# Kernel optimization log

Measured on AMD Instinct MI355X. Metric: run time of the kernel, lower is better.

## Reference

```python
import jax, jax.numpy as jnp
import numpy as np

N_HEAD = 8
D_K = 64
D_V = 512
TOP_K = 64
NEG = jnp.finfo(jnp.float32).min


def setup_inputs() -> dict:
    key = jax.random.key(0)
    ks = jax.random.split(key, 10)
    B, Lq, Lk, E = 2, 2048, 2048, 512
    q = jax.random.normal(ks[0], (B, Lq, E), dtype=jnp.float32)
    k = jax.random.normal(ks[1], (B, Lk, E), dtype=jnp.float32)
    v = jax.random.normal(ks[2], (B, Lk, D_V), dtype=jnp.float32)
    post_softmax_mask = jax.random.randint(ks[3], (B, 1, Lq, Lk), 0, 2, dtype=jnp.int32)
    query_mask_flat = jax.random.uniform(ks[4], (B, Lq), dtype=jnp.float32)
    # Linear weights stored input-major: y = x @ W
    Wq = jax.random.normal(ks[5], (E, N_HEAD * D_K), dtype=jnp.float32) * (E ** -0.5)
    Wk = jax.random.normal(ks[6], (E, N_HEAD * D_K), dtype=jnp.float32) * (E ** -0.5)
    Wv = jax.random.normal(ks[7], (D_V, N_HEAD * D_V), dtype=jnp.float32) * (D_V ** -0.5)
    Wfc = jax.random.normal(ks[8], (N_HEAD * D_V, D_V), dtype=jnp.float32) * ((N_HEAD * D_V) ** -0.5)
    return {"q": q, "k": k, "v": v, "post_softmax_mask": post_softmax_mask,
            "query_mask_flat": query_mask_flat, "Wq": Wq, "Wk": Wk, "Wv": Wv, "Wfc": Wfc}


def _topk_keep_mask(logits, top_k):
    # Scatter True at the per-row top-k indices (matches torch.topk + scatter_).
    B, H, Lq, Lk = logits.shape
    _, idx = jax.lax.top_k(logits, top_k)              # [B,H,Lq,K]
    rows = B * H * Lq
    keep = jnp.zeros((rows, Lk), dtype=bool)
    keep = keep.at[jnp.arange(rows)[:, None], idx.reshape(rows, top_k)].set(True)
    return keep.reshape(B, H, Lq, Lk)


def reference(q, k, v, post_softmax_mask, query_mask_flat, Wq, Wk, Wv, Wfc):
    B, Lq, _ = q.shape
    Lk = k.shape[1]
    q_proj = (q @ Wq).reshape(B, Lq, N_HEAD, D_K).transpose(0, 2, 1, 3)   # [B,H,Lq,dk]
    k_proj = (k @ Wk).reshape(B, Lk, N_HEAD, D_K).transpose(0, 2, 1, 3)   # [B,H,Lk,dk]
    logits = jnp.einsum('bhqd,bhkd->bhqk', q_proj * (D_K ** -0.5), k_proj).astype(jnp.float32)
    # post-softmax mask (applied pre-softmax via -inf fill, as in source)
    logits = jnp.where(post_softmax_mask == 0, NEG, logits)
    # top-k restriction, skipped for rows where query_mask_flat <= 0.5
    keep = _topk_keep_mask(logits, TOP_K)
    masked_queries = (query_mask_flat > 0.5)[:, None, :, None]            # [B,1,Lq,1]
    keep = jnp.where(masked_queries, keep, True)
    logits = jnp.where(keep, logits, NEG)
    attn_probs = jax.nn.softmax(logits, axis=-1).astype(v.dtype)          # [B,H,Lq,Lk]
    v_proj = (v @ Wv).reshape(B, Lk, N_HEAD, D_V).transpose(0, 2, 1, 3)   # [B,H,Lk,dv]
    mixed = jnp.einsum('bhqk,bhkd->bhqd', attn_probs, v_proj)
    output = mixed.transpose(0, 2, 1, 3).reshape(B, Lq, N_HEAD * D_V) @ Wfc
    return output, attn_probs
```

## Files before the change

### kernel.cpp

```cpp
#include <hip/hip_runtime.h>
#include <stdint.h>

#define NEGF  (-3.402823466e38f)
#define TOPK  64

typedef __attribute__((ext_vector_type(8))) short bfrag8;
typedef __attribute__((ext_vector_type(4))) float f32x4;
typedef __attribute__((ext_vector_type(16))) float f32x16;

static __device__ __forceinline__ unsigned short f2bf(float f) {
  union { float f; unsigned u; } c; c.f = f;
  unsigned u = c.u;
  return (unsigned short)((u + 0x7fffu + ((u >> 16) & 1u)) >> 16);
}
static __device__ __forceinline__ unsigned mono(float x) {
  union { float f; unsigned u; } c; c.f = x;
  return (c.u & 0x80000000u) ? ~c.u : (c.u | 0x80000000u);
}
static __device__ __forceinline__ float invmono(unsigned k) {
  union { unsigned u; float f; } c;
  c.u = (k & 0x80000000u) ? (k ^ 0x80000000u) : ~k;
  return c.f;
}
static __device__ __forceinline__ int waveSum(int v) {
  #pragma unroll
  for (int o = 1; o < 64; o <<= 1) v += __shfl_xor(v, o);
  return v;
}
static __device__ __forceinline__ float waveSumF(float v) {
  #pragma unroll
  for (int o = 1; o < 64; o <<= 1) v += __shfl_xor(v, o);
  return v;
}
static __device__ __forceinline__ unsigned waveMaxU(unsigned v) {
  #pragma unroll
  for (int o = 1; o < 64; o <<= 1) {
    unsigned t = (unsigned)__shfl_xor((int)v, o);
    v = v > t ? v : t;
  }
  return v;
}

template<int OBF>
__global__ __launch_bounds__(256) void transpose_k(const float* __restrict__ in,
                                                   void* __restrict__ out, int R, int C) {
  __shared__ float t[32][33];
  int c0 = blockIdx.x * 32, r0 = blockIdx.y * 32;
  int tx = threadIdx.x & 31, ty = (threadIdx.x >> 5) * 4;
  #pragma unroll
  for (int i = 0; i < 4; i++)
    t[ty + i][tx] = in[(size_t)(r0 + ty + i) * C + c0 + tx];
  __syncthreads();
  #pragma unroll
  for (int i = 0; i < 4; i++) {
    float v = t[tx][ty + i];
    size_t idx = (size_t)(c0 + ty + i) * R + r0 + tx;
    if (OBF) ((unsigned short*)out)[idx] = f2bf(v);
    else     ((float*)out)[idx] = v;
  }
}

__global__ __launch_bounds__(256) void proj_f32_kernel(
    const float* __restrict__ q, const float* __restrict__ k,
    const float* __restrict__ WqT, const float* __restrict__ WkT,
    float* __restrict__ qp, float* __restrict__ kp) {
  __shared__ float AsT[64][132];
  __shared__ float BsT[64][132];
  int tid = threadIdx.x;
  int z = blockIdx.z;
  const float* A  = z ? k : q;
  const float* Bt = z ? WkT : WqT;
  float* out      = z ? kp : qp;
  float scale     = z ? 1.0f : 0.125f;
  int m0 = blockIdx.y * 128, n0 = blockIdx.x * 128;
  int lane = tid & 63, w = tid >> 6;
  int lx = lane & 15, ly = lane >> 4;
  int ra = w * 32 + ly * 4;
  int ca = lx * 4;
  int rr = tid >> 1;
  int kq0 = (tid & 1) << 5;
  float acc[8][8] = {};
  for (int k0 = 0; k0 < 512; k0 += 64) {
    const float* ar = A  + (size_t)(m0 + rr) * 512 + k0 + kq0;
    const float* br = Bt + (size_t)(n0 + rr) * 512 + k0 + kq0;
    #pragma unroll
    for (int s = 0; s < 8; s++) {
      float4 av = *(const float4*)(ar + (s << 2));
      float4 bv = *(const float4*)(br + (s << 2));
      int kk = kq0 + (s << 2);
      AsT[kk+0][rr] = av.x; AsT[kk+1][rr] = av.y; AsT[kk+2][rr] = av.z; AsT[kk+3][rr] = av.w;
      BsT[kk+0][rr] = bv.x; BsT[kk+1][rr] = bv.y; BsT[kk+2][rr] = bv.z; BsT[kk+3][rr] = bv.w;
    }
    __syncthreads();
    #pragma unroll 2
    for (int d = 0; d < 64; d++) {
      f32x4 a0 = *(const f32x4*)&AsT[d][ra];
      f32x4 a1 = *(const f32x4*)&AsT[d][ra + 16];
      f32x4 b0 = *(const f32x4*)&BsT[d][ca];
      f32x4 b1 = *(const f32x4*)&BsT[d][ca + 64];
      float a[8] = {a0[0],a0[1],a0[2],a0[3],a1[0],a1[1],a1[2],a1[3]};
      float bb[8] = {b0[0],b0[1],b0[2],b0[3],b1[0],b1[1],b1[2],b1[3]};
      #pragma unroll
      for (int i = 0; i < 8; i++)
        #pragma unroll
        for (int j = 0; j < 8; j++)
          acc[i][j] = fmaf(a[i], bb[j], acc[i][j]);
    }
    __syncthreads();
  }
  #pragma unroll
  for (int i = 0; i < 8; i++) {
    int m = m0 + ra + (i & 3) + ((i >> 2) << 4);
    int b = m >> 11, l = m & 2047;
    #pragma unroll
    for (int half = 0; half < 2; half++) {
      int n = n0 + ca + half * 64;
      int h = n >> 6, dd = n & 63;
      float4 v4;
      v4.x = acc[i][half*4+0]*scale; v4.y = acc[i][half*4+1]*scale;
      v4.z = acc[i][half*4+2]*scale; v4.w = acc[i][half*4+3]*scale;
      *(float4*)(out + ((((size_t)b*8 + h)*2048 + l)*64 + dd)) = v4;
    }
  }
}

__global__ __launch_bounds__(256) void logits_mask_kernel(
    const float* __restrict__ qp, const float* __restrict__ kp,
    const int* __restrict__ mask, float* __restrict__ out) {
  __shared__ float AsT[64][132];
  __shared__ float BsT[64][132];
  int tid = threadIdx.x;
  int z = blockIdx.z, b = z >> 3;
  int m0 = blockIdx.y * 128, n0 = blockIdx.x * 128;
  const float* Ap = qp + (size_t)z * (2048 * 64);
  const float* Bp = kp + (size_t)z * (2048 * 64);
  {
    int rr = tid >> 2;
    int kq = (tid & 3) << 2;
    #pragma unroll
    for (int pass = 0; pass < 2; pass++) {
      int r = rr + (pass << 6);
      const float* ar = Ap + (size_t)(m0 + r) * 64 + kq;
      const float* br = Bp + (size_t)(n0 + r) * 64 + kq;
      #pragma unroll
      for (int s = 0; s < 4; s++) {
        float4 av = *(const float4*)(ar + (s << 4));
        float4 bv = *(const float4*)(br + (s << 4));
        int k = kq + (s << 4);
        AsT[k+0][r] = av.x; AsT[k+1][r] = av.y; AsT[k+2][r] = av.z; AsT[k+3][r] = av.w;
        BsT[k+0][r] = bv.x; BsT[k+1][r] = bv.y; BsT[k+2][r] = bv.z; BsT[k+3][r] = bv.w;
      }
    }
  }
  __syncthreads();
  int lane = tid & 63, w = tid >> 6;
  int lx = lane & 15, ly = lane >> 4;
  int ra = w * 32 + ly * 4;
  int ca = lx * 4;
  float acc[8][8] = {};
  #pragma unroll 2
  for (int d = 0; d < 64; d++) {
    f32x4 a0 = *(const f32x4*)&AsT[d][ra];
    f32x4 a1 = *(const f32x4*)&AsT[d][ra + 16];
    f32x4 b0 = *(const f32x4*)&BsT[d][ca];
    f32x4 b1 = *(const f32x4*)&BsT[d][ca + 64];
    float a[8] = {a0[0],a0[1],a0[2],a0[3],a1[0],a1[1],a1[2],a1[3]};
    float bb[8] = {b0[0],b0[1],b0[2],b0[3],b1[0],b1[1],b1[2],b1[3]};
    #pragma unroll
    for (int i = 0; i < 8; i++)
      #pragma unroll
      for (int j = 0; j < 8; j++)
        acc[i][j] = fmaf(a[i], bb[j], acc[i][j]);
  }
  size_t outbase = (size_t)z * 2048 * 2048;
  const int* mbase = mask + (size_t)b * 2048 * 2048;
  #pragma unroll
  for (int i = 0; i < 8; i++) {
    int row = m0 + ra + (i & 3) + ((i >> 2) << 4);
    const int* mp = mbase + (size_t)row * 2048 + n0;
    float* op = out + outbase + (size_t)row * 2048 + n0;
    int4 mv0 = *(const int4*)(mp + ca);
    int4 mv1 = *(const int4*)(mp + ca + 64);
    float4 o0, o1;
    o0.x = mv0.x ? acc[i][0] : NEGF;
    o0.y = mv0.y ? acc[i][1] : NEGF;
    o0.z = mv0.z ? acc[i][2] : NEGF;
    o0.w = mv0.w ? acc[i][3] : NEGF;
    o1.x = mv1.x ? acc[i][4] : NEGF;
    o1.y = mv1.y ? acc[i][5] : NEGF;
    o1.z = mv1.z ? acc[i][6] : NEGF;
    o1.w = mv1.w ? acc[i][7] : NEGF;
    *(float4*)(op + ca) = o0;
    *(float4*)(op + ca + 64) = o1;
  }
}

__global__ __launch_bounds__(256) void vproj_kernel(const float* __restrict__ v,
    const unsigned short* __restrict__ WvT, unsigned short* __restrict__ vpT) {
  __shared__ unsigned short As[128][64];
  __shared__ unsigned short Bs[128][64];
  int tid = threadIdx.x;
  int lane = tid & 63, wv = tid >> 6;
  int l31 = lane & 31, lh = lane >> 5;
  int wr = wv >> 1, wc = wv & 1;
  int z = blockIdx.z, b = z >> 3, h = z & 7;
  int m0 = blockIdx.y * 128, n0 = blockIdx.x * 128;
  const unsigned short* Ap = WvT + (size_t)(h * 512 + m0) * 512;
  const float* Bp = v + ((size_t)b * 2048 + n0) * 512;
  f32x16 acc[2][2];
  #pragma unroll
  for (int mf = 0; mf < 2; mf++)
    #pragma unroll
    for (int nf = 0; nf < 2; nf++)
      #pragma unroll
      for (int r = 0; r < 16; r++) acc[mf][nf][r] = 0.f;
  int srow = tid >> 1;
  int skc = (tid & 1) << 5;
  for (int k0 = 0; k0 < 512; k0 += 64) {
    {
      const bfrag8* s = (const bfrag8*)(Ap + (size_t)srow * 512 + k0 + skc);
      #pragma unroll
      for (int j = 0; j < 4; j++) {
        int c = (skc >> 3) + j;
        *(bfrag8*)&As[srow][((c + srow) & 7) * 8] = s[j];
      }
    }
    {
      const float* s = Bp + (size_t)srow * 512 + k0 + skc;
      #pragma unroll
      for (int j = 0; j < 4; j++) {
        float4 x0 = *(const float4*)(s + 8*j);
        float4 x1 = *(const float4*)(s + 8*j + 4);
        union { bfrag8 v; unsigned short u[8]; } p;
        p.u[0]=f2bf(x0.x); p.u[1]=f2bf(x0.y); p.u[2]=f2bf(x0.z); p.u[3]=f2bf(x0.w);
        p.u[4]=f2bf(x1.x); p.u[5]=f2bf(x1.y); p.u[6]=f2bf(x1.z); p.u[7]=f2bf(x1.w);
        int c = (skc >> 3) + j;
        *(bfrag8*)&Bs[srow][((c + srow) & 7) * 8] = p.v;
      }
    }
    __syncthreads();
    #pragma unroll
    for (int ks = 0; ks < 4; ks++) {
      int qd = ks * 2 + lh;
      bfrag8 af[2], bfr[2];
      #pragma unroll
      for (int mf = 0; mf < 2; mf++) {
        int r = wr * 64 + mf * 32 + l31;
        af[mf] = *(const bfrag8*)&As[r][((qd + r) & 7) * 8];
      }
      #pragma unroll
      for (int nf = 0; nf < 2; nf++) {
        int n = wc * 64 + nf * 32 + l31;
        bfr[nf] = *(const bfrag8*)&Bs[n][((qd + n) & 7) * 8];
      }
      #pragma unroll
      for (int mf = 0; mf < 2; mf++)
        #pragma unroll
        for (int nf = 0; nf < 2; nf++)
          acc[mf][nf] = __builtin_amdgcn_mfma_f32_32x32x16_bf16(af[mf], bfr[nf], acc[mf][nf], 0, 0, 0);
    }
    __syncthreads();
  }
  #pragma unroll
  for (int mf = 0; mf < 2; mf++)
    #pragma unroll
    for (int nf = 0; nf < 2; nf++) {
      int l = n0 + wc * 64 + nf * 32 + l31;
      #pragma unroll
      for (int r = 0; r < 16; r++) {
        int d = m0 + wr * 64 + mf * 32 + (r & 3) + ((r >> 2) << 3) + (lh << 2);
        vpT[((size_t)z * 512 + d) * 2048 + l] = f2bf(acc[mf][nf][r]);
      }
    }
}

__global__ __launch_bounds__(256) void gemm_bf16_fc(const unsigned short* __restrict__ A,
    const unsigned short* __restrict__ Bt, float* __restrict__ Cout,
    int M, int N, int K) {
  __shared__ unsigned short As[64][72];
  __shared__ unsigned short Bs[128][72];
  int tid = threadIdx.x;
  int lane = tid & 63, wave = tid >> 6;
  int wr = wave >> 1, wc = wave & 1;
  int m0 = blockIdx.y * 64, n0 = blockIdx.x * 128;
  f32x4 acc[2][4];
  #pragma unroll
  for (int mi = 0; mi < 2; mi++)
    #pragma unroll
    for (int ni = 0; ni < 4; ni++) acc[mi][ni] = (f32x4){0.f, 0.f, 0.f, 0.f};
  int arow = tid >> 2, akc = (tid & 3) << 4;
  int brow = tid >> 1, bkc = (tid & 1) << 5;
  for (int k0 = 0; k0 < K; k0 += 64) {
    {
      const bfrag8* s = (const bfrag8*)(A + (size_t)(m0 + arow) * K + k0 + akc);
      *(bfrag8*)&As[arow][akc + 0] = s[0];
      *(bfrag8*)&As[arow][akc + 8] = s[1];
    }
    {
      const bfrag8* s = (const bfrag8*)(Bt + (size_t)(n0 + brow) * K + k0 + bkc);
      #pragma unroll
      for (int j = 0; j < 4; j++)
        *(bfrag8*)&Bs[brow][bkc + 8*j] = s[j];
    }
    __syncthreads();
    #pragma unroll
    for (int kh = 0; kh < 2; kh++) {
      int krd = (kh << 5) + ((lane >> 4) << 3);
      bfrag8 af[2], bfr[4];
      #pragma unroll
      for (int mi = 0; mi < 2; mi++)
        af[mi] = *(const bfrag8*)&As[wr*32 + mi*16 + (lane & 15)][krd];
      #pragma unroll
      for (int ni = 0; ni < 4; ni++)
        bfr[ni] = *(const bfrag8*)&Bs[wc*64 + ni*16 + (lane & 15)][krd];
      #pragma unroll
      for (int mi = 0; mi < 2; mi++)
        #pragma unroll
        for (int ni = 0; ni < 4; ni++)
          acc[mi][ni] = __builtin_amdgcn_mfma_f32_16x16x32_bf16(af[mi], bfr[ni], acc[mi][ni], 0, 0, 0);
    }
    __syncthreads();
  }
  #pragma unroll
  for (int mi = 0; mi < 2; mi++) {
    int rb = m0 + wr*32 + mi*16 + ((lane >> 4) << 2);
    #pragma unroll
    for (int ni = 0; ni < 4; ni++) {
      int col = n0 + wc*64 + ni*16 + (lane & 15);
      f32x4 v = acc[mi][ni];
      #pragma unroll
      for (int j = 0; j < 4; j++)
        Cout[(size_t)(rb + j)*512 + col] = v[j];
    }
  }
}

__global__ __launch_bounds__(512) void pv_kernel(const float* __restrict__ probs,
    const unsigned short* __restrict__ vpT, unsigned short* __restrict__ mixed) {
  __shared__ unsigned short As[64][64];
  __shared__ unsigned short Bs[512][64];
  int tid = threadIdx.x;
  int lane = tid & 63, wv = tid >> 6;
  int l31 = lane & 31, lh = lane >> 5;
  int z = blockIdx.z, m0 = blockIdx.y * 64;
  const float* Ap = probs + (size_t)z * 2048 * 2048 + (size_t)m0 * 2048;
  const unsigned short* Bp = vpT + (size_t)z * 512 * 2048;
  f32x16 acc[2][2];
  #pragma unroll
  for (int mf = 0; mf < 2; mf++)
    #pragma unroll
    for (int nf = 0; nf < 2; nf++)
      #pragma unroll
      for (int r = 0; r < 16; r++) acc[mf][nf][r] = 0.f;
  int a_r = tid >> 3, a_c = tid & 7;
  for (int k0 = 0; k0 < 2048; k0 += 64) {
    {
      const float* s = Ap + (size_t)a_r * 2048 + k0 + a_c * 8;
      float4 x0 = *(const float4*)s;
      float4 x1 = *(const float4*)(s + 4);
      union { bfrag8 v; unsigned short u[8]; } p;
      p.u[0]=f2bf(x0.x); p.u[1]=f2bf(x0.y); p.u[2]=f2bf(x0.z); p.u[3]=f2bf(x0.w);
      p.u[4]=f2bf(x1.x); p.u[5]=f2bf(x1.y); p.u[6]=f2bf(x1.z); p.u[7]=f2bf(x1.w);
      *(bfrag8*)&As[a_r][((a_c + a_r) & 7) * 8] = p.v;
    }
    #pragma unroll
    for (int s = 0; s < 8; s++) {
      int n = (tid >> 3) + (s << 6);
      bfrag8 vb = *(const bfrag8*)(Bp + (size_t)n * 2048 + k0 + a_c * 8);
      *(bfrag8*)&Bs[n][((a_c + n) & 7) * 8] = vb;
    }
    __syncthreads();
    #pragma unroll
    for (int ks = 0; ks < 4; ks++) {
      int qd = ks * 2 + lh;
      bfrag8 af[2], bfr[2];
      #pragma unroll
      for (int mf = 0; mf < 2; mf++) {
        int r = mf * 32 + l31;
        af[mf] = *(const bfrag8*)&As[r][((qd + r) & 7) * 8];
      }
      #pragma unroll
      for (int nf = 0; nf < 2; nf++) {
        int n = wv * 64 + nf * 32 + l31;
        bfr[nf] = *(const bfrag8*)&Bs[n][((qd + n) & 7) * 8];
      }
      #pragma unroll
      for (int mf = 0; mf < 2; mf++)
        #pragma unroll
        for (int nf = 0; nf < 2; nf++)
          acc[mf][nf] = __builtin_amdgcn_mfma_f32_32x32x16_bf16(af[mf], bfr[nf], acc[mf][nf], 0, 0, 0);
    }
    __syncthreads();
  }
  int bb = z >> 3, h = z & 7;
  #pragma unroll
  for (int mf = 0; mf < 2; mf++)
    #pragma unroll
    for (int nf = 0; nf < 2; nf++) {
      int n = wv * 64 + nf * 32 + l31;
      #pragma unroll
      for (int r = 0; r < 16; r++) {
        int row = m0 + mf * 32 + (r & 3) + ((r >> 2) << 3) + (lh << 2);
        mixed[((size_t)bb * 2048 + row) * 4096 + h * 512 + n] = f2bf(acc[mf][nf][r]);
      }
    }
}

__global__ __launch_bounds__(256) void topk_softmax_k(float* __restrict__ probs,
    const float* __restrict__ qmaskf) {
  int lane = threadIdx.x & 63;
  int row = blockIdx.x * 4 + (threadIdx.x >> 6);
  int b = row >> 14, q = row & 2047;
  float* rp = probs + (size_t)row * 2048;
  unsigned key[32];
  #pragma unroll
  for (int j = 0; j < 8; j++) {
    int base = (lane << 2) + (j << 8);
    float4 v = *(const float4*)(rp + base);
    key[4*j+0] = mono(v.x);
    key[4*j+1] = mono(v.y);
    key[4*j+2] = mono(v.z);
    key[4*j+3] = mono(v.w);
  }
  unsigned drop = 0;
  bool qm = qmaskf[b * 2048 + q] > 0.5f;
  if (qm) {
    unsigned lo = 0u, hi = 0xFFFFu;
    while (lo < hi) {
      unsigned mid = lo + ((hi - lo + 1u) >> 1);
      unsigned t = mid << 16;
      int c = 0;
      #pragma unroll
      for (int e = 0; e < 32; e++) c += (key[e] >= t) ? 1 : 0;
      c = waveSum(c);
      if (c >= TOPK) lo = mid; else hi = mid - 1u;
    }
    unsigned P = lo;
    unsigned hiMax = (P << 16) | 0xFFFFu;
    int cgt_hi = 0;
    #pragma unroll
    for (int e = 0; e < 32; e++) cgt_hi += (key[e] > hiMax) ? 1 : 0;
    cgt_hi = waveSum(cgt_hi);
    int remaining = TOPK - cgt_hi;
    unsigned cur = 0xFFFFFFFFu;
    unsigned K64 = P << 16;
    for (;;) {
      unsigned mx = 0;
      #pragma unroll
      for (int e = 0; e < 32; e++) {
        unsigned kk = key[e];
        if ((kk >> 16) == P && kk < cur) mx = mx > kk ? mx : kk;
      }
      mx = waveMaxU(mx);
      int ce = 0;
      #pragma unroll
      for (int e = 0; e < 32; e++) ce += (key[e] == mx) ? 1 : 0;
      ce = waveSum(ce);
      if (remaining <= ce) { K64 = mx; break; }
      remaining -= ce;
      cur = mx;
    }
    int cgt = 0, ceq = 0;
    #pragma unroll
    for (int e = 0; e < 32; e++) { cgt += (key[e] > K64) ? 1 : 0; ceq += (key[e] == K64) ? 1 : 0; }
    cgt = waveSum(cgt);
    int ceqT = waveSum(ceq);
    int r = TOPK - cgt;
    #pragma unroll
    for (int e = 0; e < 32; e++) if (key[e] < K64) drop |= (1u << e);
    if (ceqT > r) {
      int taken = 0;
      for (int j = 0; j < 8; j++) {
        int cl = 0, eqm = 0;
        #pragma unroll
        for (int t = 0; t < 4; t++)
          if (key[4*j+t] == K64) { eqm |= (1 << t); cl++; }
        int incl = cl;
        for (int o = 1; o < 64; o <<= 1) {
          int tt = __shfl_up(incl, o);
          if (lane >= o) incl += tt;
        }
        int pref = incl - cl;
        int tot = __shfl(incl, 63);
        int rk = taken + pref;
        #pragma unroll
        for (int t = 0; t < 4; t++) {
          if ((eqm >> t) & 1) {
            if (rk >= r) drop |= (1u << (4*j+t));
            rk++;
          }
        }
        taken += tot;
      }
    }
  }
  unsigned kmax = 0;
  #pragma unroll
  for (int e = 0; e < 32; e++)
    if (!((drop >> e) & 1u)) kmax = kmax > key[e] ? kmax : key[e];
  kmax = waveMaxU(kmax);
  float mx = invmono(kmax);
  float ex[32]; float s = 0.f;
  #pragma unroll
  for (int e = 0; e < 32; e++) {
    float t = ((drop >> e) & 1u) ? 0.f : __expf(invmono(key[e]) - mx);
    ex[e] = t; s += t;
  }
  s = waveSumF(s);
  float inv = 1.0f / s;
  #pragma unroll
  for (int j = 0; j < 8; j++) {
    int base = (lane << 2) + (j << 8);
    float4 o;
    o.x = ex[4*j+0]*inv; o.y = ex[4*j+1]*inv; o.z = ex[4*j+2]*inv; o.w = ex[4*j+3]*inv;
    *(float4*)(rp + base) = o;
  }
}

extern "C" void kernel_launch(void* const* d_in, const int* in_sizes, int n_in,
                              void* d_out, int out_size, void* d_ws, size_t ws_size,
                              hipStream_t stream) {
  (void)in_sizes; (void)n_in; (void)out_size; (void)ws_size;
  const float* q     = (const float*)d_in[0];
  const float* k     = (const float*)d_in[1];
  const float* v     = (const float*)d_in[2];
  const int*   mask  = (const int*)d_in[3];
  const float* qmask = (const float*)d_in[4];
  const float* Wq    = (const float*)d_in[5];
  const float* Wk    = (const float*)d_in[6];
  const float* Wv    = (const float*)d_in[7];
  const float* Wfc   = (const float*)d_in[8];

  float* out   = (float*)d_out;
  float* probs = out + 2097152;

  char* ws = (char*)d_ws;
  float*          qp    = (float*)(ws + 0);
  float*          kp    = (float*)(ws + 8388608);
  unsigned short* vpT   = (unsigned short*)(ws + 16777216);
  unsigned short* mixed = (unsigned short*)(ws + 50331648);
  float*          WqT   = (float*)(ws + 83886080);
  float*          WkT   = (float*)(ws + 84934656);
  unsigned short* WvT   = (unsigned short*)(ws + 85983232);
  unsigned short* WfcT  = (unsigned short*)(ws + 90177536);

  transpose_k<0><<<dim3(16, 16),  256, 0, stream>>>(Wq,  WqT,  512, 512);
  transpose_k<0><<<dim3(16, 16),  256, 0, stream>>>(Wk,  WkT,  512, 512);
  transpose_k<1><<<dim3(128, 16), 256, 0, stream>>>(Wv,  WvT,  512, 4096);
  transpose_k<1><<<dim3(16, 128), 256, 0, stream>>>(Wfc, WfcT, 4096, 512);

  proj_f32_kernel<<<dim3(4, 32, 2), 256, 0, stream>>>(q, k, WqT, WkT, qp, kp);

  vproj_kernel<<<dim3(16, 4, 16), 256, 0, stream>>>(v, WvT, vpT);

  logits_mask_kernel<<<dim3(16, 16, 16), 256, 0, stream>>>(qp, kp, mask, probs);

  topk_softmax_k<<<dim3(8192), 256, 0, stream>>>(probs, qmask);

  pv_kernel<<<dim3(1, 32, 16), 512, 0, stream>>>(probs, vpT, mixed);

  gemm_bf16_fc<<<dim3(4, 64), 256, 0, stream>>>(mixed, WfcT, out, 4096, 512, 4096);
}
```

Baseline: 581.0 us.

## Retile PV kernel with register prefetch, use hardware bf16 pack and ballot counts

The PV kernel's block tile grows to 128 rows across 512 columns, with a 2x4 wave grid and XCD-aware block remapping. Global loads for the next K tile are prefetched into registers while the current tile computes, which removes one barrier per iteration. Software bf16 rounding is replaced by the v_cvt_pk_bf16_f32 instruction in the PV and fc kernels. The top-k kernel uses ballot+popcount counts instead of shuffle reductions and recomputes exp rather than keeping a 32-entry array. The FMA loops in the projection and logits kernels are reordered and unrolled further. The bigger tiles and prefetch registers raise register and LDS pressure, which may limit occupancy.

Result: no change. 591.6 us (+1.8%).

```diff
diff --git a/kernel.cpp b/kernel.cpp
--- a/kernel.cpp
+++ b/kernel.cpp
@@ -13,6 +13,11 @@
   unsigned u = c.u;
   return (unsigned short)((u + 0x7fffu + ((u >> 16) & 1u)) >> 16);
 }
+static __device__ __forceinline__ unsigned cvtpk_bf16(float lo, float hi) {
+  unsigned r;
+  asm("v_cvt_pk_bf16_f32 %0, %1, %2" : "=v"(r) : "v"(lo), "v"(hi));
+  return r;
+}
 static __device__ __forceinline__ unsigned mono(float x) {
   union { float f; unsigned u; } c; c.f = x;
   return (c.u & 0x80000000u) ? ~c.u : (c.u | 0x80000000u);
@@ -21,11 +26,6 @@
   union { unsigned u; float f; } c;
   c.u = (k & 0x80000000u) ? (k ^ 0x80000000u) : ~k;
   return c.f;
-}
-static __device__ __forceinline__ int waveSum(int v) {
-  #pragma unroll
-  for (int o = 1; o < 64; o <<= 1) v += __shfl_xor(v, o);
-  return v;
 }
 static __device__ __forceinline__ float waveSumF(float v) {
   #pragma unroll
@@ -92,19 +92,22 @@
       BsT[kk+0][rr] = bv.x; BsT[kk+1][rr] = bv.y; BsT[kk+2][rr] = bv.z; BsT[kk+3][rr] = bv.w;
     }
     __syncthreads();
-    #pragma unroll 2
+    #pragma unroll 4
     for (int d = 0; d < 64; d++) {
       f32x4 a0 = *(const f32x4*)&AsT[d][ra];
       f32x4 a1 = *(const f32x4*)&AsT[d][ra + 16];
       f32x4 b0 = *(const f32x4*)&BsT[d][ca];
       f32x4 b1 = *(const f32x4*)&BsT[d][ca + 64];
-      float a[8] = {a0[0],a0[1],a0[2],a0[3],a1[0],a1[1],a1[2],a1[3]};
-      float bb[8] = {b0[0],b0[1],b0[2],b0[3],b1[0],b1[1],b1[2],b1[3]};
-      #pragma unroll
-      for (int i = 0; i < 8; i++)
+      #pragma unroll
+      for (int i = 0; i < 4; i++) {
         #pragma unroll
-        for (int j = 0; j < 8; j++)
-          acc[i][j] = fmaf(a[i], bb[j], acc[i][j]);
+        for (int j = 0; j < 4; j++) {
+          acc[i][j]     = fmaf(a0[i], b0[j], acc[i][j]);
+          acc[i][j+4]   = fmaf(a0[i], b1[j], acc[i][j+4]);
+          acc[i+4][j]   = fmaf(a1[i], b0[j], acc[i+4][j]);
+          acc[i+4][j+4] = fmaf(a1[i], b1[j], acc[i+4][j+4]);
+        }
+      }
     }
     __syncthreads();
   }
@@ -158,19 +161,22 @@
   int ra = w * 32 + ly * 4;
   int ca = lx * 4;
   float acc[8][8] = {};
-  #pragma unroll 2
+  #pragma unroll 4
   for (int d = 0; d < 64; d++) {
     f32x4 a0 = *(const f32x4*)&AsT[d][ra];
     f32x4 a1 = *(const f32x4*)&AsT[d][ra + 16];
     f32x4 b0 = *(const f32x4*)&BsT[d][ca];
     f32x4 b1 = *(const f32x4*)&BsT[d][ca + 64];
-    float a[8] = {a0[0],a0[1],a0[2],a0[3],a1[0],a1[1],a1[2],a1[3]};
-    float bb[8] = {b0[0],b0[1],b0[2],b0[3],b1[0],b1[1],b1[2],b1[3]};
-    #pragma unroll
-    for (int i = 0; i < 8; i++)
-      #pragma unroll
-      for (int j = 0; j < 8; j++)
-        acc[i][j] = fmaf(a[i], bb[j], acc[i][j]);
+    #pragma unroll
+    for (int i = 0; i < 4; i++) {
+      #pragma unroll
+      for (int j = 0; j < 4; j++) {
+        acc[i][j]     = fmaf(a0[i], b0[j], acc[i][j]);
+        acc[i][j+4]   = fmaf(a0[i], b1[j], acc[i][j+4]);
+        acc[i+4][j]   = fmaf(a1[i], b0[j], acc[i+4][j]);
+        acc[i+4][j+4] = fmaf(a1[i], b1[j], acc[i+4][j+4]);
+      }
+    }
   }
   size_t outbase = (size_t)z * 2048 * 2048;
   const int* mbase = mask + (size_t)b * 2048 * 2048;
@@ -231,9 +237,9 @@
       for (int j = 0; j < 4; j++) {
         float4 x0 = *(const float4*)(s + 8*j);
         float4 x1 = *(const float4*)(s + 8*j + 4);
-        union { bfrag8 v; unsigned short u[8]; } p;
-        p.u[0]=f2bf(x0.x); p.u[1]=f2bf(x0.y); p.u[2]=f2bf(x0.z); p.u[3]=f2bf(x0.w);
-        p.u[4]=f2bf(x1.x); p.u[5]=f2bf(x1.y); p.u[6]=f2bf(x1.z); p.u[7]=f2bf(x1.w);
+        union { bfrag8 v; unsigned w[4]; } p;
+        p.w[0] = cvtpk_bf16(x0.x, x0.y); p.w[1] = cvtpk_bf16(x0.z, x0.w);
+        p.w[2] = cvtpk_bf16(x1.x, x1.y); p.w[3] = cvtpk_bf16(x1.z, x1.w);
         int c = (skc >> 3) + j;
         *(bfrag8*)&Bs[srow][((c + srow) & 7) * 8] = p.v;
       }
@@ -335,72 +341,104 @@
   }
 }
 
-__global__ __launch_bounds__(512) void pv_kernel(const float* __restrict__ probs,
+__global__ __launch_bounds__(512, 2) void pv_kernel(const float* __restrict__ probs,
     const unsigned short* __restrict__ vpT, unsigned short* __restrict__ mixed) {
-  __shared__ unsigned short As[64][64];
+  __shared__ unsigned short As[128][64];
   __shared__ unsigned short Bs[512][64];
   int tid = threadIdx.x;
   int lane = tid & 63, wv = tid >> 6;
   int l31 = lane & 31, lh = lane >> 5;
-  int z = blockIdx.z, m0 = blockIdx.y * 64;
+  int wr = wv >> 2, wc = wv & 3;
+  int bid = blockIdx.y + (blockIdx.z << 4);
+  int xcd = bid & 7, idx = bid >> 3;
+  int z = (xcd << 1) + (idx >> 4);
+  int m0 = (idx & 15) << 7;
   const float* Ap = probs + (size_t)z * 2048 * 2048 + (size_t)m0 * 2048;
   const unsigned short* Bp = vpT + (size_t)z * 512 * 2048;
-  f32x16 acc[2][2];
+  f32x16 acc[2][4];
   #pragma unroll
   for (int mf = 0; mf < 2; mf++)
     #pragma unroll
-    for (int nf = 0; nf < 2; nf++)
+    for (int nf = 0; nf < 4; nf++)
       #pragma unroll
       for (int r = 0; r < 16; r++) acc[mf][nf][r] = 0.f;
-  int a_r = tid >> 3, a_c = tid & 7;
-  for (int k0 = 0; k0 < 2048; k0 += 64) {
+  int a_r = tid >> 2, a_c = tid & 3;
+  float4 ra0, ra1, ra2, ra3;
+  bfrag8 rb[8];
+  const float* abase = Ap + (size_t)a_r * 2048 + a_c * 16;
+  const unsigned short* bbase = Bp + (size_t)(tid >> 2) * 2048 + a_c * 16;
+
+  {
+    const float* s = abase;
+    ra0 = *(const float4*)(s); ra1 = *(const float4*)(s + 4);
+    ra2 = *(const float4*)(s + 8); ra3 = *(const float4*)(s + 12);
+    #pragma unroll
+    for (int s4 = 0; s4 < 4; s4++) {
+      const bfrag8* bs = (const bfrag8*)(bbase + ((size_t)s4 << 18));
+      rb[2*s4]   = bs[0];
+      rb[2*s4+1] = bs[1];
+    }
+  }
+  for (int kt = 0; kt < 32; kt++) {
+    if (kt) __syncthreads();
     {
-      const float* s = Ap + (size_t)a_r * 2048 + k0 + a_c * 8;
-      float4 x0 = *(const float4*)s;
-      float4 x1 = *(const float4*)(s + 4);
-      union { bfrag8 v; unsigned short u[8]; } p;
-      p.u[0]=f2bf(x0.x); p.u[1]=f2bf(x0.y); p.u[2]=f2bf(x0.z); p.u[3]=f2bf(x0.w);
-      p.u[4]=f2bf(x1.x); p.u[5]=f2bf(x1.y); p.u[6]=f2bf(x1.z); p.u[7]=f2bf(x1.w);
-      *(bfrag8*)&As[a_r][((a_c + a_r) & 7) * 8] = p.v;
-    }
-    #pragma unroll
-    for (int s = 0; s < 8; s++) {
-      int n = (tid >> 3) + (s << 6);
-      bfrag8 vb = *(const bfrag8*)(Bp + (size_t)n * 2048 + k0 + a_c * 8);
-      *(bfrag8*)&Bs[n][((a_c + n) & 7) * 8] = vb;
+      union { bfrag8 v; unsigned w[4]; } p0, p1;
+      p0.w[0] = cvtpk_bf16(ra0.x, ra0.y); p0.w[1] = cvtpk_bf16(ra0.z, ra0.w);
+      p0.w[2] = cvtpk_bf16(ra1.x, ra1.y); p0.w[3] = cvtpk_bf16(ra1.z, ra1.w);
+      p1.w[0] = cvtpk_bf16(ra2.x, ra2.y); p1.w[1] = cvtpk_bf16(ra2.z, ra2.w);
+      p1.w[2] = cvtpk_bf16(ra3.x, ra3.y); p1.w[3] = cvtpk_bf16(ra3.z, ra3.w);
+      int c0 = 2 * a_c;
+      *(bfrag8*)&As[a_r][((c0 + a_r) & 7) * 8]     = p0.v;
+      *(bfrag8*)&As[a_r][((c0 + 1 + a_r) & 7) * 8] = p1.v;
+      #pragma unroll
+      for (int s4 = 0; s4 < 4; s4++) {
+        int n = (tid >> 2) + (s4 << 7);
+        *(bfrag8*)&Bs[n][((c0 + n) & 7) * 8]     = rb[2*s4];
+        *(bfrag8*)&Bs[n][((c0 + 1 + n) & 7) * 8] = rb[2*s4+1];
+      }
     }
     __syncthreads();
+    if (kt < 31) {
+      const float* s = abase + (kt + 1) * 64;
+      ra0 = *(const float4*)(s); ra1 = *(const float4*)(s + 4);
+      ra2 = *(const float4*)(s + 8); ra3 = *(const float4*)(s + 12);
+      #pragma unroll
+      for (int s4 = 0; s4 < 4; s4++) {
+        const bfrag8* bs = (const bfrag8*)(bbase + ((size_t)s4 << 18) + (kt + 1) * 64);
+        rb[2*s4]   = bs[0];
+        rb[2*s4+1] = bs[1];
+      }
+    }
     #pragma unroll
     for (int ks = 0; ks < 4; ks++) {
       int qd = ks * 2 + lh;
-      bfrag8 af[2], bfr[2];
+      bfrag8 af[2], bfr[4];
       #pragma unroll
       for (int mf = 0; mf < 2; mf++) {
-        int r = mf * 32 + l31;
+        int r = wr * 64 + mf * 32 + l31;
         af[mf] = *(const bfrag8*)&As[r][((qd + r) & 7) * 8];
       }
       #pragma unroll
-      for (int nf = 0; nf < 2; nf++) {
-        int n = wv * 64 + nf * 32 + l31;
+      for (int nf = 0; nf < 4; nf++) {
+        int n = wc * 128 + nf * 32 + l31;
         bfr[nf] = *(const bfrag8*)&Bs[n][((qd + n) & 7) * 8];
       }
       #pragma unroll
       for (int mf = 0; mf < 2; mf++)
         #pragma unroll
-        for (int nf = 0; nf < 2; nf++)
+        for (int nf = 0; nf < 4; nf++)
           acc[mf][nf] = __builtin_amdgcn_mfma_f32_32x32x16_bf16(af[mf], bfr[nf], acc[mf][nf], 0, 0, 0);
     }
-    __syncthreads();
   }
   int bb = z >> 3, h = z & 7;
   #pragma unroll
   for (int mf = 0; mf < 2; mf++)
     #pragma unroll
-    for (int nf = 0; nf < 2; nf++) {
-      int n = wv * 64 + nf * 32 + l31;
+    for (int nf = 0; nf < 4; nf++) {
+      int n = wc * 128 + nf * 32 + l31;
       #pragma unroll
       for (int r = 0; r < 16; r++) {
-        int row = m0 + mf * 32 + (r & 3) + ((r >> 2) << 3) + (lh << 2);
+        int row = m0 + wr * 64 + mf * 32 + (r & 3) + ((r >> 2) << 3) + (lh << 2);
         mixed[((size_t)bb * 2048 + row) * 4096 + h * 512 + n] = f2bf(acc[mf][nf][r]);
       }
     }
@@ -431,16 +469,14 @@
       unsigned t = mid << 16;
       int c = 0;
       #pragma unroll
-      for (int e = 0; e < 32; e++) c += (key[e] >= t) ? 1 : 0;
-      c = waveSum(c);
+      for (int e = 0; e < 32; e++) c += __popcll(__ballot(key[e] >= t));
       if (c >= TOPK) lo = mid; else hi = mid - 1u;
     }
     unsigned P = lo;
     unsigned hiMax = (P << 16) | 0xFFFFu;
     int cgt_hi = 0;
     #pragma unroll
-    for (int e = 0; e < 32; e++) cgt_hi += (key[e] > hiMax) ? 1 : 0;
-    cgt_hi = waveSum(cgt_hi);
+    for (int e = 0; e < 32; e++) cgt_hi += __popcll(__ballot(key[e] > hiMax));
     int remaining = TOPK - cgt_hi;
     unsigned cur = 0xFFFFFFFFu;
     unsigned K64 = P << 16;
@@ -454,17 +490,17 @@
       mx = waveMaxU(mx);
       int ce = 0;
       #pragma unroll
-      for (int e = 0; e < 32; e++) ce += (key[e] == mx) ? 1 : 0;
-      ce = waveSum(ce);
+      for (int e = 0; e < 32; e++) ce += __popcll(__ballot(key[e] == mx));
       if (remaining <= ce) { K64 = mx; break; }
       remaining -= ce;
       cur = mx;
     }
-    int cgt = 0, ceq = 0;
-    #pragma unroll
-    for (int e = 0; e < 32; e++) { cgt += (key[e] > K64) ? 1 : 0; ceq += (key[e] == K64) ? 1 : 0; }
-    cgt = waveSum(cgt);
-    int ceqT = waveSum(ceq);
+    int cgt = 0, ceqT = 0;
+    #pragma unroll
+    for (int e = 0; e < 32; e++) {
+      cgt  += __popcll(__ballot(key[e] > K64));
+      ceqT += __popcll(__ballot(key[e] == K64));
+    }
     int r = TOPK - cgt;
     #pragma unroll
     for (int e = 0; e < 32; e++) if (key[e] < K64) drop |= (1u << e);
@@ -500,19 +536,20 @@
     if (!((drop >> e) & 1u)) kmax = kmax > key[e] ? kmax : key[e];
   kmax = waveMaxU(kmax);
   float mx = invmono(kmax);
-  float ex[32]; float s = 0.f;
-  #pragma unroll
-  for (int e = 0; e < 32; e++) {
-    float t = ((drop >> e) & 1u) ? 0.f : __expf(invmono(key[e]) - mx);
-    ex[e] = t; s += t;
-  }
+  float s = 0.f;
+  #pragma unroll
+  for (int e = 0; e < 32; e++)
+    if (!((drop >> e) & 1u)) s += __expf(invmono(key[e]) - mx);
   s = waveSumF(s);
   float inv = 1.0f / s;
   #pragma unroll
   for (int j = 0; j < 8; j++) {
     int base = (lane << 2) + (j << 8);
     float4 o;
-    o.x = ex[4*j+0]*inv; o.y = ex[4*j+1]*inv; o.z = ex[4*j+2]*inv; o.w = ex[4*j+3]*inv;
+    o.x = ((drop >> (4*j+0)) & 1u) ? 0.f : __expf(invmono(key[4*j+0]) - mx) * inv;
+    o.y = ((drop >> (4*j+1)) & 1u) ? 0.f : __expf(invmono(key[4*j+1]) - mx) * inv;
+    o.z = ((drop >> (4*j+2)) & 1u) ? 0.f : __expf(invmono(key[4*j+2]) - mx) * inv;
+    o.w = ((drop >> (4*j+3)) & 1u) ? 0.f : __expf(invmono(key[4*j+3]) - mx) * inv;
     *(float4*)(rp + base) = o;
   }
 }
@@ -557,7 +594,7 @@
 
   topk_softmax_k<<<dim3(8192), 256, 0, stream>>>(probs, qmask);
 
-  pv_kernel<<<dim3(1, 32, 16), 512, 0, stream>>>(probs, vpT, mixed);
+  pv_kernel<<<dim3(1, 16, 16), 512, 0, stream>>>(probs, vpT, mixed);
 
   gemm_bf16_fc<<<dim3(4, 64), 256, 0, stream>>>(mixed, WfcT, out, 4096, 512, 4096);
 }
```

## Bit-pack mask, ballot-based topk counts, packed bf16 cvt, XCD-aware pv mapping

Applied to the files above, without the earlier changes.

Several independent changes land together. A new kernel packs the int32 mask into bits so the logits kernel reads one word per 32 mask entries instead of re-reading the full mask for every head. The topk kernel uses ballot/popcount instead of shuffle reductions for its counts, and recomputes exp at store time instead of holding 32 values in registers. It also converts to bf16 with v_cvt_pk_bf16_f32 inline asm, adds unroll 4 with restructured FMA loops in the fp32 GEMMs, and remaps pv_kernel blocks so each XCD handles two heads for L2 locality. The extra pack pass still reads the 32 MB mask once, and v_cvt_pk_bf16 may round differently from the manual code.

Result: slower. 620.1 us (+6.7%).

```diff
diff --git a/kernel.cpp b/kernel.cpp
--- a/kernel.cpp
+++ b/kernel.cpp
@@ -13,6 +13,11 @@
   unsigned u = c.u;
   return (unsigned short)((u + 0x7fffu + ((u >> 16) & 1u)) >> 16);
 }
+static __device__ __forceinline__ unsigned cvtpk_bf16(float lo, float hi) {
+  unsigned r;
+  asm("v_cvt_pk_bf16_f32 %0, %1, %2" : "=v"(r) : "v"(lo), "v"(hi));
+  return r;
+}
 static __device__ __forceinline__ unsigned mono(float x) {
   union { float f; unsigned u; } c; c.f = x;
   return (c.u & 0x80000000u) ? ~c.u : (c.u | 0x80000000u);
@@ -21,11 +26,6 @@
   union { unsigned u; float f; } c;
   c.u = (k & 0x80000000u) ? (k ^ 0x80000000u) : ~k;
   return c.f;
-}
-static __device__ __forceinline__ int waveSum(int v) {
-  #pragma unroll
-  for (int o = 1; o < 64; o <<= 1) v += __shfl_xor(v, o);
-  return v;
 }
 static __device__ __forceinline__ float waveSumF(float v) {
   #pragma unroll
@@ -58,6 +58,15 @@
     if (OBF) ((unsigned short*)out)[idx] = f2bf(v);
     else     ((float*)out)[idx] = v;
   }
+}
+
+__global__ __launch_bounds__(256) void mask_pack_kernel(const int* __restrict__ mask,
+    unsigned* __restrict__ mpack) {
+  size_t idx = (size_t)blockIdx.x * 256 + threadIdx.x;
+  int lane = threadIdx.x & 63;
+  unsigned long long bal = __ballot(mask[idx] != 0);
+  if (lane == 0)       mpack[idx >> 5] = (unsigned)bal;
+  else if (lane == 32) mpack[idx >> 5] = (unsigned)(bal >> 32);
 }
 
 __global__ __launch_bounds__(256) void proj_f32_kernel(
@@ -92,19 +101,22 @@
       BsT[kk+0][rr] = bv.x; BsT[kk+1][rr] = bv.y; BsT[kk+2][rr] = bv.z; BsT[kk+3][rr] = bv.w;
     }
     __syncthreads();
-    #pragma unroll 2
+    #pragma unroll 4
     for (int d = 0; d < 64; d++) {
       f32x4 a0 = *(const f32x4*)&AsT[d][ra];
       f32x4 a1 = *(const f32x4*)&AsT[d][ra + 16];
       f32x4 b0 = *(const f32x4*)&BsT[d][ca];
       f32x4 b1 = *(const f32x4*)&BsT[d][ca + 64];
-      float a[8] = {a0[0],a0[1],a0[2],a0[3],a1[0],a1[1],a1[2],a1[3]};
-      float bb[8] = {b0[0],b0[1],b0[2],b0[3],b1[0],b1[1],b1[2],b1[3]};
-      #pragma unroll
-      for (int i = 0; i < 8; i++)
+      #pragma unroll
+      for (int i = 0; i < 4; i++) {
         #pragma unroll
-        for (int j = 0; j < 8; j++)
-          acc[i][j] = fmaf(a[i], bb[j], acc[i][j]);
+        for (int j = 0; j < 4; j++) {
+          acc[i][j]     = fmaf(a0[i], b0[j], acc[i][j]);
+          acc[i][j+4]   = fmaf(a0[i], b1[j], acc[i][j+4]);
+          acc[i+4][j]   = fmaf(a1[i], b0[j], acc[i+4][j]);
+          acc[i+4][j+4] = fmaf(a1[i], b1[j], acc[i+4][j+4]);
+        }
+      }
     }
     __syncthreads();
   }
@@ -126,7 +138,7 @@
 
 __global__ __launch_bounds__(256) void logits_mask_kernel(
     const float* __restrict__ qp, const float* __restrict__ kp,
-    const int* __restrict__ mask, float* __restrict__ out) {
+    const unsigned* __restrict__ mpack, float* __restrict__ out) {
   __shared__ float AsT[64][132];
   __shared__ float BsT[64][132];
   int tid = threadIdx.x;
@@ -158,40 +170,148 @@
   int ra = w * 32 + ly * 4;
   int ca = lx * 4;
   float acc[8][8] = {};
-  #pragma unroll 2
+  #pragma unroll 4
   for (int d = 0; d < 64; d++) {
     f32x4 a0 = *(const f32x4*)&AsT[d][ra];
     f32x4 a1 = *(const f32x4*)&AsT[d][ra + 16];
     f32x4 b0 = *(const f32x4*)&BsT[d][ca];
     f32x4 b1 = *(const f32x4*)&BsT[d][ca + 64];
-    float a[8] = {a0[0],a0[1],a0[2],a0[3],a1[0],a1[1],a1[2],a1[3]};
-    float bb[8] = {b0[0],b0[1],b0[2],b0[3],b1[0],b1[1],b1[2],b1[3]};
-    #pragma unroll
-    for (int i = 0; i < 8; i++)
-      #pragma unroll
-      for (int j = 0; j < 8; j++)
-        acc[i][j] = fmaf(a[i], bb[j], acc[i][j]);
+    #pragma unroll
+    for (int i = 0; i < 4; i++) {
+      #pragma unroll
+      for (int j = 0; j < 4; j++) {
+        acc[i][j]     = fmaf(a0[i], b0[j], acc[i][j]);
+        acc[i][j+4]   = fmaf(a0[i], b1[j], acc[i][j+4]);
+        acc[i+4][j]   = fmaf(a1[i], b0[j], acc[i+4][j]);
+        acc[i+4][j+4] = fmaf(a1[i], b1[j], acc[i+4][j+4]);
+      }
+    }
   }
   size_t outbase = (size_t)z * 2048 * 2048;
-  const int* mbase = mask + (size_t)b * 2048 * 2048;
+  const unsigned* mpb = mpack + (size_t)b * 2048 * 64;
+  int w0i = (n0 + ca) >> 5, s0 = ca & 31;
+  int w1i = (n0 + ca + 64) >> 5;
   #pragma unroll
   for (int i = 0; i < 8; i++) {
     int row = m0 + ra + (i & 3) + ((i >> 2) << 4);
-    const int* mp = mbase + (size_t)row * 2048 + n0;
+    const unsigned* mpr = mpb + (size_t)row * 64;
     float* op = out + outbase + (size_t)row * 2048 + n0;
-    int4 mv0 = *(const int4*)(mp + ca);
-    int4 mv1 = *(const int4*)(mp + ca + 64);
+    unsigned nib0 = (mpr[w0i] >> s0) & 0xFu;
+    unsigned nib1 = (mpr[w1i] >> s0) & 0xFu;
     float4 o0, o1;
-    o0.x = mv0.x ? acc[i][0] : NEGF;
-    o0.y = mv0.y ? acc[i][1] : NEGF;
-    o0.z = mv0.z ? acc[i][2] : NEGF;
-    o0.w = mv0.w ? acc[i][3] : NEGF;
-    o1.x = mv1.x ? acc[i][4] : NEGF;
-    o1.y = mv1.y ? acc[i][5] : NEGF;
-    o1.z = mv1.z ? acc[i][6] : NEGF;
-    o1.w = mv1.w ? acc[i][7] : NEGF;
+    o0.x = (nib0 & 1u) ? acc[i][0] : NEGF;
+    o0.y = (nib0 & 2u) ? acc[i][1] : NEGF;
+    o0.z = (nib0 & 4u) ? acc[i][2] : NEGF;
+    o0.w = (nib0 & 8u) ? acc[i][3] : NEGF;
+    o1.x = (nib1 & 1u) ? acc[i][4] : NEGF;
+    o1.y = (nib1 & 2u) ? acc[i][5] : NEGF;
+    o1.z = (nib1 & 4u) ? acc[i][6] : NEGF;
+    o1.w = (nib1 & 8u) ? acc[i][7] : NEGF;
     *(float4*)(op + ca) = o0;
     *(float4*)(op + ca + 64) = o1;
+  }
+}
+
+__global__ __launch_bounds__(256) void topk_softmax_k(float* __restrict__ probs,
+    const float* __restrict__ qmaskf) {
+  int lane = threadIdx.x & 63;
+  int row = blockIdx.x * 4 + (threadIdx.x >> 6);
+  int b = row >> 14, q = row & 2047;
+  float* rp = probs + (size_t)row * 2048;
+  unsigned key[32];
+  #pragma unroll
+  for (int j = 0; j < 8; j++) {
+    int base = (lane << 2) + (j << 8);
+    float4 v = *(const float4*)(rp + base);
+    key[4*j+0] = mono(v.x);
+    key[4*j+1] = mono(v.y);
+    key[4*j+2] = mono(v.z);
+    key[4*j+3] = mono(v.w);
+  }
+  unsigned drop = 0;
+  bool qm = qmaskf[b * 2048 + q] > 0.5f;
+  if (qm) {
+    unsigned lo = 0u, hi = 0xFFFFu;
+    while (lo < hi) {
+      unsigned mid = lo + ((hi - lo + 1u) >> 1);
+      unsigned t = mid << 16;
+      int c = 0;
+      #pragma unroll
+      for (int e = 0; e < 32; e++) c += __popcll(__ballot(key[e] >= t));
+      if (c >= TOPK) lo = mid; else hi = mid - 1u;
+    }
+    unsigned P = lo;
+    unsigned hiMax = (P << 16) | 0xFFFFu;
+    int cgt_hi = 0;
+    #pragma unroll
+    for (int e = 0; e < 32; e++) cgt_hi += __popcll(__ballot(key[e] > hiMax));
+    int remaining = TOPK - cgt_hi;
+    unsigned cur = 0xFFFFFFFFu;
+    unsigned K64 = P << 16;
+    for (;;) {
+      unsigned mx = 0;
+      #pragma unroll
+      for (int e = 0; e < 32; e++) {
+        unsigned kk = key[e];
+        if ((kk >> 16) == P && kk < cur) mx = mx > kk ? mx : kk;
+      }
+      mx = waveMaxU(mx);
+      int ce = 0;
+      #pragma unroll
+      for (int e = 0; e < 32; e++) ce += __popcll(__ballot(key[e] == mx));
+      if (remaining <= ce) { K64 = mx; break; }
+      remaining -= ce;
+      cur = mx;
+    }
+    int cgt = 0, ceqT = 0;
+    #pragma unroll
+    for (int e = 0; e < 32; e++) {
+      cgt  += __popcll(__ballot(key[e] > K64));
+      ceqT += __popcll(__ballot(key[e] == K64));
+    }
+    int r = TOPK - cgt;
+    #pragma unroll
+    for (int e = 0; e < 32; e++) if (key[e] < K64) drop |= (1u << e);
+    if (ceqT > r) {
+      int taken = 0;
+      unsigned long long ltm = (1ull << lane) - 1ull;
+      for (int j = 0; j < 8; ++j) {
+        bool e0 = key[4*j+0] == K64, e1 = key[4*j+1] == K64;
+        bool e2 = key[4*j+2] == K64, e3 = key[4*j+3] == K64;
+        unsigned long long bb0 = __ballot(e0), bb1 = __ballot(e1);
+        unsigned long long bb2 = __ballot(e2), bb3 = __ballot(e3);
+        int below = __popcll(bb0 & ltm) + __popcll(bb1 & ltm)
+                  + __popcll(bb2 & ltm) + __popcll(bb3 & ltm);
+        int base = taken + below, o = 0;
+        if (e0) { if (base + o >= r) drop |= (1u << (4*j+0)); o++; }
+        if (e1) { if (base + o >= r) drop |= (1u << (4*j+1)); o++; }
+        if (e2) { if (base + o >= r) drop |= (1u << (4*j+2)); o++; }
+        if (e3) { if (base + o >= r) drop |= (1u << (4*j+3)); o++; }
+        taken += __popcll(bb0) + __popcll(bb1) + __popcll(bb2) + __popcll(bb3);
+      }
+    }
+  }
+  unsigned kmax = 0;
+  #pragma unroll
+  for (int e = 0; e < 32; e++)
+    if (!((drop >> e) & 1u)) kmax = kmax > key[e] ? kmax : key[e];
+  kmax = waveMaxU(kmax);
+  float mx = invmono(kmax);
+  float s = 0.f;
+  #pragma unroll
+  for (int e = 0; e < 32; e++)
+    if (!((drop >> e) & 1u)) s += __expf(invmono(key[e]) - mx);
+  s = waveSumF(s);
+  float inv = 1.0f / s;
+  #pragma unroll
+  for (int j = 0; j < 8; j++) {
+    int base = (lane << 2) + (j << 8);
+    float4 o;
+    o.x = ((drop >> (4*j+0)) & 1u) ? 0.f : __expf(invmono(key[4*j+0]) - mx) * inv;
+    o.y = ((drop >> (4*j+1)) & 1u) ? 0.f : __expf(invmono(key[4*j+1]) - mx) * inv;
+    o.z = ((drop >> (4*j+2)) & 1u) ? 0.f : __expf(invmono(key[4*j+2]) - mx) * inv;
+    o.w = ((drop >> (4*j+3)) & 1u) ? 0.f : __expf(invmono(key[4*j+3]) - mx) * inv;
+    *(float4*)(rp + base) = o;
   }
 }
 
@@ -231,9 +351,9 @@
       for (int j = 0; j < 4; j++) {
         float4 x0 = *(const float4*)(s + 8*j);
         float4 x1 = *(const float4*)(s + 8*j + 4);
-        union { bfrag8 v; unsigned short u[8]; } p;
-        p.u[0]=f2bf(x0.x); p.u[1]=f2bf(x0.y); p.u[2]=f2bf(x0.z); p.u[3]=f2bf(x0.w);
-        p.u[4]=f2bf(x1.x); p.u[5]=f2bf(x1.y); p.u[6]=f2bf(x1.z); p.u[7]=f2bf(x1.w);
+        union { bfrag8 v; unsigned w[4]; } p;
+        p.w[0] = cvtpk_bf16(x0.x, x0.y); p.w[1] = cvtpk_bf16(x0.z, x0.w);
+        p.w[2] = cvtpk_bf16(x1.x, x1.y); p.w[3] = cvtpk_bf16(x1.z, x1.w);
         int c = (skc >> 3) + j;
         *(bfrag8*)&Bs[srow][((c + srow) & 7) * 8] = p.v;
       }
@@ -342,7 +462,10 @@
   int tid = threadIdx.x;
   int lane = tid & 63, wv = tid >> 6;
   int l31 = lane & 31, lh = lane >> 5;
-  int z = blockIdx.z, m0 = blockIdx.y * 64;
+  int bid = blockIdx.x;
+  int xcd = bid & 7, idx = bid >> 3;
+  int z = (xcd << 1) | (idx >> 5);
+  int m0 = (idx & 31) << 6;
   const float* Ap = probs + (size_t)z * 2048 * 2048 + (size_t)m0 * 2048;
   const unsigned short* Bp = vpT + (size_t)z * 512 * 2048;
   f32x16 acc[2][2];
@@ -358,9 +481,9 @@
       const float* s = Ap + (size_t)a_r * 2048 + k0 + a_c * 8;
       float4 x0 = *(const float4*)s;
       float4 x1 = *(const float4*)(s + 4);
-      union { bfrag8 v; unsigned short u[8]; } p;
-      p.u[0]=f2bf(x0.x); p.u[1]=f2bf(x0.y); p.u[2]=f2bf(x0.z); p.u[3]=f2bf(x0.w);
-      p.u[4]=f2bf(x1.x); p.u[5]=f2bf(x1.y); p.u[6]=f2bf(x1.z); p.u[7]=f2bf(x1.w);
+      union { bfrag8 v; unsigned w[4]; } p;
+      p.w[0] = cvtpk_bf16(x0.x, x0.y); p.w[1] = cvtpk_bf16(x0.z, x0.w);
+      p.w[2] = cvtpk_bf16(x1.x, x1.y); p.w[3] = cvtpk_bf16(x1.z, x1.w);
       *(bfrag8*)&As[a_r][((a_c + a_r) & 7) * 8] = p.v;
     }
     #pragma unroll
@@ -404,117 +527,6 @@
         mixed[((size_t)bb * 2048 + row) * 4096 + h * 512 + n] = f2bf(acc[mf][nf][r]);
       }
     }
-}
-
-__global__ __launch_bounds__(256) void topk_softmax_k(float* __restrict__ probs,
-    const float* __restrict__ qmaskf) {
-  int lane = threadIdx.x & 63;
-  int row = blockIdx.x * 4 + (threadIdx.x >> 6);
-  int b = row >> 14, q = row & 2047;
-  float* rp = probs + (size_t)row * 2048;
-  unsigned key[32];
-  #pragma unroll
-  for (int j = 0; j < 8; j++) {
-    int base = (lane << 2) + (j << 8);
-    float4 v = *(const float4*)(rp + base);
-    key[4*j+0] = mono(v.x);
-    key[4*j+1] = mono(v.y);
-    key[4*j+2] = mono(v.z);
-    key[4*j+3] = mono(v.w);
-  }
-  unsigned drop = 0;
-  bool qm = qmaskf[b * 2048 + q] > 0.5f;
-  if (qm) {
-    unsigned lo = 0u, hi = 0xFFFFu;
-    while (lo < hi) {
-      unsigned mid = lo + ((hi - lo + 1u) >> 1);
-      unsigned t = mid << 16;
-      int c = 0;
-      #pragma unroll
-      for (int e = 0; e < 32; e++) c += (key[e] >= t) ? 1 : 0;
-      c = waveSum(c);
-      if (c >= TOPK) lo = mid; else hi = mid - 1u;
-    }
-    unsigned P = lo;
-    unsigned hiMax = (P << 16) | 0xFFFFu;
-    int cgt_hi = 0;
-    #pragma unroll
-    for (int e = 0; e < 32; e++) cgt_hi += (key[e] > hiMax) ? 1 : 0;
-    cgt_hi = waveSum(cgt_hi);
-    int remaining = TOPK - cgt_hi;
-    unsigned cur = 0xFFFFFFFFu;
-    unsigned K64 = P << 16;
-    for (;;) {
-      unsigned mx = 0;
-      #pragma unroll
-      for (int e = 0; e < 32; e++) {
-        unsigned kk = key[e];
-        if ((kk >> 16) == P && kk < cur) mx = mx > kk ? mx : kk;
-      }
-      mx = waveMaxU(mx);
-      int ce = 0;
-      #pragma unroll
-      for (int e = 0; e < 32; e++) ce += (key[e] == mx) ? 1 : 0;
-      ce = waveSum(ce);
-      if (remaining <= ce) { K64 = mx; break; }
-      remaining -= ce;
-      cur = mx;
-    }
-    int cgt = 0, ceq = 0;
-    #pragma unroll
-    for (int e = 0; e < 32; e++) { cgt += (key[e] > K64) ? 1 : 0; ceq += (key[e] == K64) ? 1 : 0; }
-    cgt = waveSum(cgt);
-    int ceqT = waveSum(ceq);
-    int r = TOPK - cgt;
-    #pragma unroll
-    for (int e = 0; e < 32; e++) if (key[e] < K64) drop |= (1u << e);
-    if (ceqT > r) {
-      int taken = 0;
-      for (int j = 0; j < 8; j++) {
-        int cl = 0, eqm = 0;
-        #pragma unroll
-        for (int t = 0; t < 4; t++)
-          if (key[4*j+t] == K64) { eqm |= (1 << t); cl++; }
-        int incl = cl;
-        for (int o = 1; o < 64; o <<= 1) {
-          int tt = __shfl_up(incl, o);
-          if (lane >= o) incl += tt;
-        }
-        int pref = incl - cl;
-        int tot = __shfl(incl, 63);
-        int rk = taken + pref;
-        #pragma unroll
-        for (int t = 0; t < 4; t++) {
-          if ((eqm >> t) & 1) {
-            if (rk >= r) drop |= (1u << (4*j+t));
-            rk++;
-          }
-        }
-        taken += tot;
-      }
-    }
-  }
-  unsigned kmax = 0;
-  #pragma unroll
-  for (int e = 0; e < 32; e++)
-    if (!((drop >> e) & 1u)) kmax = kmax > key[e] ? kmax : key[e];
-  kmax = waveMaxU(kmax);
-  float mx = invmono(kmax);
-  float ex[32]; float s = 0.f;
-  #pragma unroll
-  for (int e = 0; e < 32; e++) {
-    float t = ((drop >> e) & 1u) ? 0.f : __expf(invmono(key[e]) - mx);
-    ex[e] = t; s += t;
-  }
-  s = waveSumF(s);
-  float inv = 1.0f / s;
-  #pragma unroll
-  for (int j = 0; j < 8; j++) {
-    int base = (lane << 2) + (j << 8);
-    float4 o;
-    o.x = ex[4*j+0]*inv; o.y = ex[4*j+1]*inv; o.z = ex[4*j+2]*inv; o.w = ex[4*j+3]*inv;
-    *(float4*)(rp + base) = o;
-  }
 }
 
 extern "C" void kernel_launch(void* const* d_in, const int* in_sizes, int n_in,
@@ -539,6 +551,7 @@
   float*          kp    = (float*)(ws + 8388608);
   unsigned short* vpT   = (unsigned short*)(ws + 16777216);
   unsigned short* mixed = (unsigned short*)(ws + 50331648);
+  unsigned*       mpack = (unsigned*)(ws + 58720256);
   float*          WqT   = (float*)(ws + 83886080);
   float*          WkT   = (float*)(ws + 84934656);
   unsigned short* WvT   = (unsigned short*)(ws + 85983232);
@@ -549,15 +562,17 @@
   transpose_k<1><<<dim3(128, 16), 256, 0, stream>>>(Wv,  WvT,  512, 4096);
   transpose_k<1><<<dim3(16, 128), 256, 0, stream>>>(Wfc, WfcT, 4096, 512);
 
+  mask_pack_kernel<<<dim3(32768), 256, 0, stream>>>(mask, mpack);
+
   proj_f32_kernel<<<dim3(4, 32, 2), 256, 0, stream>>>(q, k, WqT, WkT, qp, kp);
 
   vproj_kernel<<<dim3(16, 4, 16), 256, 0, stream>>>(v, WvT, vpT);
 
-  logits_mask_kernel<<<dim3(16, 16, 16), 256, 0, stream>>>(qp, kp, mask, probs);
+  logits_mask_kernel<<<dim3(16, 16, 16), 256, 0, stream>>>(qp, kp, mpack, probs);
 
   topk_softmax_k<<<dim3(8192), 256, 0, stream>>>(probs, qmask);
 
-  pv_kernel<<<dim3(1, 32, 16), 512, 0, stream>>>(probs, vpT, mixed);
+  pv_kernel<<<dim3(512), 512, 0, stream>>>(probs, vpT, mixed);
 
   gemm_bf16_fc<<<dim3(4, 64), 256, 0, stream>>>(mixed, WfcT, out, 4096, 512, 4096);
 }
```
